# Optimization experiments

Measured on AMD Instinct MI355X. Metric: run time of the kernel, lower is better.

Reference implementation:

```python
import jax, jax.numpy as jnp
import numpy as np

B, S, D_MODEL, N_HEADS, D_K, D_V = 2, 2048, 1024, 16, 64, 64
LN_EPS = 1e-5


def setup_inputs() -> dict:
    key = jax.random.key(0)
    ks = jax.random.split(key, 10)
    scale = 1.0 / np.sqrt(D_MODEL)
    inp = {
        "input_Q": jax.random.normal(ks[0], (B, S, D_MODEL), jnp.float32),
        "input_K": jax.random.normal(ks[1], (B, S, D_MODEL), jnp.float32),
        "input_V": jax.random.normal(ks[2], (B, S, D_MODEL), jnp.float32),
        # causal mask (True = masked), as produced by attn_mask() with no pad tokens
        "attn_mask": jnp.broadcast_to(
            jnp.triu(jnp.ones((S, S), dtype=bool), k=1), (B, S, S)
        ),
        # weights stored [in, out] (equivalent to torch Linear weight.T)
        "W_Q": jax.random.normal(ks[3], (D_MODEL, N_HEADS * D_K), jnp.float32) * scale,
        "W_K": jax.random.normal(ks[4], (D_MODEL, N_HEADS * D_K), jnp.float32) * scale,
        "W_V": jax.random.normal(ks[5], (D_MODEL, N_HEADS * D_V), jnp.float32) * scale,
        "W_O": jax.random.normal(ks[6], (N_HEADS * D_V, D_MODEL), jnp.float32) * scale,
        "ln_gamma": jnp.ones((D_MODEL,), jnp.float32),
        "ln_beta": jnp.zeros((D_MODEL,), jnp.float32),
    }
    return inp


def _layernorm(x, gamma, beta):
    mu = jnp.mean(x, axis=-1, keepdims=True)
    var = jnp.var(x, axis=-1, keepdims=True)
    return (x - mu) * jax.lax.rsqrt(var + LN_EPS) * gamma + beta


def reference(input_Q, input_K, input_V, attn_mask, W_Q, W_K, W_V, W_O, ln_gamma, ln_beta):
    b = input_Q.shape[0]
    # projections -> [B, H, S, d]
    Q = (input_Q @ W_Q).reshape(b, -1, N_HEADS, D_K).transpose(0, 2, 1, 3)
    K = (input_K @ W_K).reshape(b, -1, N_HEADS, D_K).transpose(0, 2, 1, 3)
    V = (input_V @ W_V).reshape(b, -1, N_HEADS, D_V).transpose(0, 2, 1, 3)
    scores = jnp.einsum("bhqd,bhkd->bhqk", Q, K) / np.sqrt(D_K)
    scores = jnp.where(attn_mask[:, None, :, :], jnp.float32(-1e9), scores)
    attn = jax.nn.softmax(scores, axis=-1)
    context = jnp.einsum("bhqk,bhkd->bhqd", attn, V)
    context = context.transpose(0, 2, 1, 3).reshape(b, -1, N_HEADS * D_V)
    output = context @ W_O
    out = _layernorm(output + input_Q, ln_gamma, ln_beta)
    return out, attn
```

## Files before the change

### kernel.cpp

```cpp
#include <hip/hip_runtime.h>
#include <stdint.h>

typedef unsigned short u16;
typedef __attribute__((ext_vector_type(8))) short short8;
typedef __attribute__((ext_vector_type(4))) float f32x4;
typedef __attribute__((ext_vector_type(4))) unsigned short u16x4;
typedef __attribute__((ext_vector_type(4))) unsigned int uint4v;

#define MFMA16(a,b,c) __builtin_amdgcn_mfma_f32_16x16x32_bf16((a),(b),(c),0,0,0)

__device__ __forceinline__ void gload16(const void* g, void* l) {
  __builtin_amdgcn_global_load_lds(
      (__attribute__((address_space(1))) void*)(uintptr_t)(g),
      (__attribute__((address_space(3))) void*)(uint32_t)(uintptr_t)(l),
      16, 0, 0);
}

__device__ __forceinline__ u16 f2bf(float x) {
  union { float f; unsigned u; } v; v.f = x;
  unsigned r = v.u + 0x7fffu + ((v.u >> 16) & 1u);
  return (u16)(r >> 16);
}
__device__ __forceinline__ unsigned pack2(float a, float b) {
  return (unsigned)f2bf(a) | ((unsigned)f2bf(b) << 16);
}

__global__ __launch_bounds__(256) void prep_kernel(const float* x0, const float* x1, const float* x2,
                                                   u16* y0, u16* y1, u16* y2,
                                                   const float* w0, const float* w1, const float* w2, const float* w3,
                                                   u16* t0, u16* t1, u16* t2, u16* t3) {
  __shared__ float tile[32][33];
  int z = blockIdx.y;
  if (z < 3) {
    const float* x = (z == 0) ? x0 : ((z == 1) ? x1 : x2);
    u16*         y = (z == 0) ? y0 : ((z == 1) ? y1 : y2);
    size_t i = ((size_t)blockIdx.x * 256 + threadIdx.x) * 4;
    float4 v = *(const float4*)(x + i);
    u16x4 o; o[0] = f2bf(v.x); o[1] = f2bf(v.y); o[2] = f2bf(v.z); o[3] = f2bf(v.w);
    *(u16x4*)(y + i) = o;
  } else {
    if (blockIdx.x >= 1024) return;
    const float* W; u16* T;
    switch (z - 3) {
      case 0:  W = w0; T = t0; break;
      case 1:  W = w1; T = t1; break;
      case 2:  W = w2; T = t2; break;
      default: W = w3; T = t3; break;
    }
    int k0 = (blockIdx.x >> 5) * 32, n0 = (blockIdx.x & 31) * 32;
    int tx = threadIdx.x & 31, ty = threadIdx.x >> 5;
#pragma unroll
    for (int j = 0; j < 4; ++j)
      tile[ty + 8*j][tx] = W[(size_t)(k0 + ty + 8*j) * 1024 + n0 + tx];
    __syncthreads();
#pragma unroll
    for (int j = 0; j < 4; ++j)
      T[(size_t)(n0 + ty + 8*j) * 1024 + k0 + tx] = f2bf(tile[tx][ty + 8*j]);
  }
}

__device__ __forceinline__ void gemm_stage(const u16* A, const u16* BT, int row0, int col0,
                                           int tid, int w, int kt, char* la, char* lb) {
#pragma unroll
  for (int j = 0; j < 2; ++j) {
    int c = j * 256 + tid;
    int mr = c & 127, kc = c >> 7;
    gload16(A  + (size_t)(row0 + mr) * 1024 + kt*32 + kc*8, la + (j*4 + w) * 1024);
    gload16(BT + (size_t)(col0 + mr) * 1024 + kt*32 + kc*8, lb + (j*4 + w) * 1024);
  }
}

__device__ __forceinline__ void gemm_core(const u16* A, const u16* BT, int row0, int col0,
                                          char* ldsA, char* ldsB, f32x4 (&acc)[4][4]) {
  int tid = threadIdx.x, w = tid >> 6, lane = tid & 63;
  int u = lane >> 4, c16 = lane & 15, wr = w >> 1, wc = w & 1;
  gemm_stage(A, BT, row0, col0, tid, w, 0, ldsA, ldsB);
  gemm_stage(A, BT, row0, col0, tid, w, 1, ldsA + 8192, ldsB + 8192);
  int cur = 0;
  for (int kt = 0; kt < 32; ++kt) {
    if (kt < 31) asm volatile("s_waitcnt vmcnt(4)" ::: "memory");
    else         asm volatile("s_waitcnt vmcnt(0)" ::: "memory");
    __builtin_amdgcn_s_barrier();
    asm volatile("" ::: "memory");
    if (kt < 30) {
      int nb = cur + 2; if (nb >= 3) nb -= 3;
      gemm_stage(A, BT, row0, col0, tid, w, kt + 2, ldsA + nb*8192, ldsB + nb*8192);
    }
    __builtin_amdgcn_sched_barrier(0);
    const char* la = ldsA + cur * 8192;
    const char* lb = ldsB + cur * 8192;
    short8 af[4], bv[4];
#pragma unroll
    for (int i = 0; i < 4; ++i) {
      af[i] = *(const short8*)(la + (u*128 + wr*64 + i*16 + c16) * 16);
      bv[i] = *(const short8*)(lb + (u*128 + wc*64 + i*16 + c16) * 16);
    }
#pragma unroll
    for (int i = 0; i < 4; ++i)
#pragma unroll
      for (int n = 0; n < 4; ++n)
        acc[i][n] = MFMA16(af[i], bv[n], acc[i][n]);
    cur = cur + 1; if (cur >= 3) cur = 0;
  }
}

__global__ __launch_bounds__(256) void gemm_qkv(const u16* Xq, const u16* Xk, const u16* Xv,
                                                const u16* WTq, const u16* WTk, const u16* WTv,
                                                u16* Qh, u16* Kh, u16* VhT) {
  __shared__ char ldsA[24576], ldsB[24576];
  int z = blockIdx.z;
  const u16* A  = (z == 0) ? Xq  : ((z == 1) ? Xk  : Xv);
  const u16* BT = (z == 0) ? WTq : ((z == 1) ? WTk : WTv);
  int row0 = blockIdx.x * 128, col0 = blockIdx.y * 128;
  f32x4 acc[4][4] = {};
  gemm_core(A, BT, row0, col0, ldsA, ldsB, acc);
  int tid = threadIdx.x, w = tid >> 6, lane = tid & 63, u = lane >> 4, c16 = lane & 15;
  int wr = w >> 1, wc = w & 1;
#pragma unroll
  for (int i = 0; i < 4; ++i)
#pragma unroll
    for (int n = 0; n < 4; ++n)
#pragma unroll
      for (int r = 0; r < 4; ++r) {
        int row = row0 + wr*64 + i*16 + u*4 + r;
        int colg = col0 + wc*64 + n*16 + c16;
        int b = row >> 11, s = row & 2047;
        int h = colg >> 6, d = colg & 63;
        float v = acc[i][n][r];
        if (z == 0)      Qh[((size_t)(b*16 + h) * 2048 + s) * 64 + d] = f2bf(v * 0.125f);
        else if (z == 1) Kh[((size_t)(b*16 + h) * 2048 + s) * 64 + d] = f2bf(v);
        else             VhT[((size_t)(b*16 + h) * 64 + d) * 2048 + s] = f2bf(v);
      }
}

__global__ __launch_bounds__(256) void gemm_out(const u16* Ctx, const u16* WTo,
                                                const float* resid, float* outF) {
  __shared__ char ldsA[24576], ldsB[24576];
  int row0 = blockIdx.x * 128, col0 = blockIdx.y * 128;
  f32x4 acc[4][4] = {};
  gemm_core(Ctx, WTo, row0, col0, ldsA, ldsB, acc);
  int tid = threadIdx.x, w = tid >> 6, lane = tid & 63, u = lane >> 4, c16 = lane & 15;
  int wr = w >> 1, wc = w & 1;
#pragma unroll
  for (int i = 0; i < 4; ++i)
#pragma unroll
    for (int n = 0; n < 4; ++n)
#pragma unroll
      for (int r = 0; r < 4; ++r) {
        int row = row0 + wr*64 + i*16 + u*4 + r;
        int colg = col0 + wc*64 + n*16 + c16;
        size_t idx = (size_t)row * 1024 + colg;
        outF[idx] = acc[i][n][r] + resid[idx];
      }
}

__device__ __forceinline__ void qk_tile(const char* Kbuf, short8 qf0, short8 qf1,
                                        int cq, int u, int rho, f32x4 (&acc)[4]) {
#pragma unroll
  for (int st = 0; st < 4; ++st) {
    short8 a0 = *(const short8*)(Kbuf + (st*16 + cq) * 128 + ((u*16) ^ rho));
    short8 a1 = *(const short8*)(Kbuf + (st*16 + cq) * 128 + ((64 + u*16) ^ rho));
    acc[st] = MFMA16(a0, qf0, acc[st]);
    acc[st] = MFMA16(a1, qf1, acc[st]);
  }
}

__device__ __forceinline__ void stage_k64(const u16* pan, int kt, char* buf, int tid, int w) {
#pragma unroll
  for (int j = 0; j < 2; ++j) {
    int c = j * 256 + tid;
    int row = c >> 3;
    int cc = (c & 7) ^ (row & 7);
    gload16(pan + (size_t)(kt*64 + row) * 64 + cc*8, buf + (j*4 + w) * 1024);
  }
}
__device__ __forceinline__ void stage_v64(const u16* vpan, int kt, char* buf, int tid, int w) {
#pragma unroll
  for (int j = 0; j < 2; ++j) {
    int c = j * 256 + tid;
    int d = c >> 3;
    int cc = (c & 7) ^ (d & 7);
    gload16(vpan + (size_t)d * 2048 + kt*64 + cc*8, buf + (j*4 + w) * 1024);
  }
}

__device__ __forceinline__ void tile_pass1(const char* Kcur, short8 qf0, short8 qf1,
                                           int q, int q0t, int kt, int ktd_t,
                                           int cq, int u, int rho, float& ls) {
  f32x4 acc[4] = {};
  qk_tile(Kcur, qf0, qf1, cq, u, rho, acc);
  if (kt == ktd_t) {
#pragma unroll
    for (int st = 0; st < 4; ++st)
#pragma unroll
      for (int r = 0; r < 4; ++r) {
        int key = q0t + st*16 + u*4 + r;
        if (key > q) acc[st][r] = -1e30f;
      }
  }
#pragma unroll
  for (int st = 0; st < 4; ++st)
#pragma unroll
    for (int r = 0; r < 4; ++r) ls += __expf(acc[st][r]);
}

__device__ __forceinline__ void tile_pass2(const char* Kcur, const char* Vcur, float* Pw,
                                           short8 qf0, short8 qf1, int q, int q0t, int kt, int ktd_t,
                                           float rl, float* apan, int w, int u, int cq,
                                           int rho, int sw, f32x4 (&ctx)[4]) {
  f32x4 acc[4] = {};
  __builtin_amdgcn_s_setprio(1);
  qk_tile(Kcur, qf0, qf1, cq, u, rho, acc);
  if (kt == ktd_t) {
#pragma unroll
    for (int st = 0; st < 4; ++st)
#pragma unroll
      for (int r = 0; r < 4; ++r) {
        int key = q0t + st*16 + u*4 + r;
        if (key > q) acc[st][r] = -1e30f;
      }
  }
#pragma unroll
  for (int st = 0; st < 4; ++st) {
    f32x4 p;
#pragma unroll
    for (int r = 0; r < 4; ++r) p[r] = __expf(acc[st][r]) * rl;
    *(f32x4*)&Pw[(cq*64 + st*16 + u*4) ^ sw] = p;
  }
  __builtin_amdgcn_sched_barrier(0);
#pragma unroll
  for (int j = 0; j < 4; ++j) {
    int row = j*4 + u;
    f32x4 v = *(const f32x4*)&Pw[(row*64 + cq*4) ^ ((row & 7) << 2)];
    __builtin_nontemporal_store(v,
        (f32x4*)(apan + (size_t)(q0t + w*16 + row) * 2048 + kt*64 + cq*4));
  }
#pragma unroll
  for (int wd = 0; wd < 2; ++wd) {
    int b0 = (cq*64 + wd*32 + u*8) ^ sw;
    f32x4 pa0 = *(const f32x4*)&Pw[b0];
    f32x4 pa1 = *(const f32x4*)&Pw[b0 ^ 4];
    uint4v pk;
    pk[0] = pack2(pa0[0], pa0[1]);
    pk[1] = pack2(pa0[2], pa0[3]);
    pk[2] = pack2(pa1[0], pa1[1]);
    pk[3] = pack2(pa1[2], pa1[3]);
    union { uint4v u4; short8 s8; } cvt; cvt.u4 = pk;
    short8 pa = cvt.s8;
#pragma unroll
    for (int nt = 0; nt < 4; ++nt) {
      short8 vb = *(const short8*)(Vcur + (nt*16 + cq) * 128 + ((wd*64 + u*16) ^ rho));
      ctx[nt] = MFMA16(pa, vb, ctx[nt]);
    }
  }
  __builtin_amdgcn_s_setprio(0);
  __builtin_amdgcn_sched_barrier(0);
}

__global__ __launch_bounds__(256) void attn_fused(const u16* Qh, const u16* Kh, const u16* VhT,
                                                  float* attnO, u16* Ctx) {
  __shared__ char Kl[2][8192];
  __shared__ char Vl[2][8192];
  __shared__ float Pf[4][1024];
  int tid = threadIdx.x, w = tid >> 6, lane = tid & 63;
  int u = lane >> 4, cq = lane & 15;
  int pi = blockIdx.x;
  int bh = blockIdx.y;
  int tlo = pi, thi = 31 - pi;
  int q0lo = tlo * 64, q0hi = thi * 64;
  int qlo = q0lo + w*16 + cq;
  int qhi = q0hi + w*16 + cq;
  int rho = (cq & 7) << 4;
  int sw  = (cq & 7) << 2;
  const u16* Kpan = Kh  + (size_t)bh * (2048 * 64);
  const u16* Vpan = VhT + (size_t)bh * (64 * 2048);
  const u16* Qlo = Qh + ((size_t)bh * 2048 + qlo) * 64;
  const u16* Qhi = Qh + ((size_t)bh * 2048 + qhi) * 64;
  short8 qlo0 = *(const short8*)(Qlo + u*8);
  short8 qlo1 = *(const short8*)(Qlo + 32 + u*8);
  short8 qhi0 = *(const short8*)(Qhi + u*8);
  short8 qhi1 = *(const short8*)(Qhi + 32 + u*8);
  float* apan = attnO + (size_t)bh * 2048 * 2048;
  int nlo = 31 - tlo;
  f32x4 z4 = {};

  float ls_lo = 0.f, ls_hi = 0.f;
  stage_k64(Kpan, 0, Kl[0], tid, w);
  for (int kt = 0; kt <= thi; ++kt) {
    int cur = kt & 1;
    if (kt == 0 || kt > 16)  asm volatile("s_waitcnt vmcnt(0)" ::: "memory");
    else if (kt <= 15)       asm volatile("s_waitcnt vmcnt(8)" ::: "memory");
    else                     asm volatile("s_waitcnt vmcnt(4)" ::: "memory");
    __builtin_amdgcn_s_barrier();
    asm volatile("" ::: "memory");
    if (kt < thi) stage_k64(Kpan, kt + 1, Kl[cur ^ 1], tid, w);
    int ns = (kt < 15) ? 8 : ((kt == 15) ? 4 : 0);
    for (int s = 0; s < ns; ++s) {
      int zidx = kt * 8 + s;
      int t = zidx >> 2, j = zidx & 3;
      int ktz, q0t;
      if (t < nlo) { ktz = tlo + 1 + t;         q0t = q0lo; }
      else         { ktz = thi + 1 + (t - nlo); q0t = q0hi; }
      __builtin_nontemporal_store(z4,
          (f32x4*)(apan + (size_t)(q0t + w*16 + j*4 + u) * 2048 + ktz*64 + cq*4));
    }
    __builtin_amdgcn_sched_barrier(0);
    __builtin_amdgcn_s_setprio(1);
    tile_pass1(Kl[cur], qhi0, qhi1, qhi, q0hi, kt, thi, cq, u, rho, ls_hi);
    if (kt <= tlo)
      tile_pass1(Kl[cur], qlo0, qlo1, qlo, q0lo, kt, tlo, cq, u, rho, ls_lo);
    __builtin_amdgcn_s_setprio(0);
  }
  ls_lo += __shfl_xor(ls_lo, 16);  ls_lo += __shfl_xor(ls_lo, 32);
  ls_hi += __shfl_xor(ls_hi, 16);  ls_hi += __shfl_xor(ls_hi, 32);
  float rl_lo = 1.f / ls_lo, rl_hi = 1.f / ls_hi;

  asm volatile("" ::: "memory");
  __builtin_amdgcn_s_barrier();
  asm volatile("" ::: "memory");

  f32x4 ctx_lo[4] = {}, ctx_hi[4] = {};
  float* Pw = Pf[w];
  stage_k64(Kpan, 0, Kl[0], tid, w);
  stage_v64(Vpan, 0, Vl[0], tid, w);
  asm volatile("s_waitcnt vmcnt(0)" ::: "memory");
  __builtin_amdgcn_s_barrier();
  asm volatile("" ::: "memory");
  for (int kt = 0; kt <= thi; ++kt) {
    int cur = kt & 1;
    if (kt < thi) {
      stage_k64(Kpan, kt + 1, Kl[cur ^ 1], tid, w);
      stage_v64(Vpan, kt + 1, Vl[cur ^ 1], tid, w);
    }
    __builtin_amdgcn_sched_barrier(0);
    tile_pass2(Kl[cur], Vl[cur], Pw, qhi0, qhi1, qhi, q0hi, kt, thi,
               rl_hi, apan, w, u, cq, rho, sw, ctx_hi);
    bool lo_act = (kt <= tlo);
    if (lo_act)
      tile_pass2(Kl[cur], Vl[cur], Pw, qlo0, qlo1, qlo, q0lo, kt, tlo,
                 rl_lo, apan, w, u, cq, rho, sw, ctx_lo);
    if (kt < thi) {
      if (lo_act) asm volatile("s_waitcnt vmcnt(8)" ::: "memory");
      else        asm volatile("s_waitcnt vmcnt(4)" ::: "memory");
      __builtin_amdgcn_s_barrier();
      asm volatile("" ::: "memory");
    }
  }

  int b = bh >> 4, h = bh & 15;
#pragma unroll
  for (int nt = 0; nt < 4; ++nt)
#pragma unroll
    for (int r = 0; r < 4; ++r) {
      int qr = q0lo + w*16 + u*4 + r;
      Ctx[((size_t)b * 2048 + qr) * 1024 + h*64 + nt*16 + cq] = f2bf(ctx_lo[nt][r]);
    }
#pragma unroll
  for (int nt = 0; nt < 4; ++nt)
#pragma unroll
    for (int r = 0; r < 4; ++r) {
      int qr = q0hi + w*16 + u*4 + r;
      Ctx[((size_t)b * 2048 + qr) * 1024 + h*64 + nt*16 + cq] = f2bf(ctx_hi[nt][r]);
    }
}

__global__ __launch_bounds__(256) void ln_kernel(const float* X, const float* g, const float* b, float* out) {
  int row = blockIdx.x, tid = threadIdx.x;
  float4 v = *(const float4*)(X + (size_t)row * 1024 + tid * 4);
  float s  = v.x + v.y + v.z + v.w;
  float q2 = v.x*v.x + v.y*v.y + v.z*v.z + v.w*v.w;
#pragma unroll
  for (int off = 32; off; off >>= 1) { s += __shfl_xor(s, off); q2 += __shfl_xor(q2, off); }
  __shared__ float red[8];
  int w = tid >> 6, lane = tid & 63;
  if (lane == 0) { red[w] = s; red[4 + w] = q2; }
  __syncthreads();
  s  = red[0] + red[1] + red[2] + red[3];
  q2 = red[4] + red[5] + red[6] + red[7];
  float mean = s * (1.f / 1024.f);
  float var  = q2 * (1.f / 1024.f) - mean * mean;
  float rs   = rsqrtf(var + 1e-5f);
  float4 gv = *(const float4*)(g + tid * 4);
  float4 bv = *(const float4*)(b + tid * 4);
  float4 o;
  o.x = (v.x - mean) * rs * gv.x + bv.x;
  o.y = (v.y - mean) * rs * gv.y + bv.y;
  o.z = (v.z - mean) * rs * gv.z + bv.z;
  o.w = (v.w - mean) * rs * gv.w + bv.w;
  *(float4*)(out + (size_t)row * 1024 + tid * 4) = o;
}

extern "C" void kernel_launch(void* const* d_in, const int* in_sizes, int n_in,
                              void* d_out, int out_size, void* d_ws, size_t ws_size,
                              hipStream_t stream) {
  (void)in_sizes; (void)n_in; (void)out_size; (void)ws_size;
  const float* inQ = (const float*)d_in[0];
  const float* inK = (const float*)d_in[1];
  const float* inV = (const float*)d_in[2];
  const float* Wq  = (const float*)d_in[4];
  const float* Wk  = (const float*)d_in[5];
  const float* Wv  = (const float*)d_in[6];
  const float* Wo  = (const float*)d_in[7];
  const float* gam = (const float*)d_in[8];
  const float* bet = (const float*)d_in[9];
  float* out   = (float*)d_out;
  float* attnO = out + (size_t)4194304;

  char* ws = (char*)d_ws;
  u16*   WTo    = (u16*)ws;
  u16*   Qh     = (u16*)(ws + 2097152);
  u16*   Kh     = (u16*)(ws + 2097152 + (size_t)8388608);
  u16*   VhT    = (u16*)(ws + 2097152 + (size_t)2*8388608);
  u16*   Ctx    = (u16*)(ws + 2097152 + (size_t)3*8388608);
  float* OutLin = (float*)(ws + 2097152 + (size_t)4*8388608);

  u16* Xbq = (u16*)attnO;
  u16* Xbk = Xbq + (size_t)4194304;
  u16* Xbv = Xbk + (size_t)4194304;
  u16* WTq = Xbv + (size_t)4194304;
  u16* WTk = WTq + (size_t)1048576;
  u16* WTv = WTk + (size_t)1048576;

  prep_kernel<<<dim3(4096, 7), 256, 0, stream>>>(inQ, inK, inV, Xbq, Xbk, Xbv,
                                                 Wq, Wk, Wv, Wo, WTq, WTk, WTv, WTo);
  gemm_qkv<<<dim3(32, 8, 3), 256, 0, stream>>>(Xbq, Xbk, Xbv, WTq, WTk, WTv, Qh, Kh, VhT);
  attn_fused<<<dim3(16, 32), 256, 0, stream>>>(Qh, Kh, VhT, attnO, Ctx);
  gemm_out<<<dim3(32, 8), 256, 0, stream>>>(Ctx, WTo, inQ, OutLin);
  ln_kernel<<<4096, 256, 0, stream>>>(OutLin, gam, bet, out);
}
```

Baseline: 270.8 us.

## Split softmax row-sum pass into separate kernel and triple-buffer attention loads

The first pass of the fused attention kernel (row sums of exp of scores, plus zero-filling the masked attn region) moves into its own kernel that writes row sums to a workspace buffer. The second pass reads those sums and now uses a three-stage K/V buffer with prefetch two tiles ahead, using computed vmcnt waits. The QKV GEMM also writes the transposed V output as packed 4-element vector stores. The aim is shorter per-kernel critical paths and better latency hiding. The cost is an extra launch, a second read of Q and K, and more LDS, which may lower occupancy.

After: 287.1 us. +6.0%, slower.

```diff
diff --git a/kernel.cpp b/kernel.cpp
--- a/kernel.cpp
+++ b/kernel.cpp
@@ -8,6 +8,7 @@
 typedef __attribute__((ext_vector_type(4))) unsigned int uint4v;
 
 #define MFMA16(a,b,c) __builtin_amdgcn_mfma_f32_16x16x32_bf16((a),(b),(c),0,0,0)
+#define VWAIT(n) asm volatile("s_waitcnt vmcnt(" #n ")" ::: "memory")
 
 __device__ __forceinline__ void gload16(const void* g, void* l) {
   __builtin_amdgcn_global_load_lds(
@@ -78,8 +79,8 @@
   gemm_stage(A, BT, row0, col0, tid, w, 1, ldsA + 8192, ldsB + 8192);
   int cur = 0;
   for (int kt = 0; kt < 32; ++kt) {
-    if (kt < 31) asm volatile("s_waitcnt vmcnt(4)" ::: "memory");
-    else         asm volatile("s_waitcnt vmcnt(0)" ::: "memory");
+    if (kt < 31) VWAIT(4);
+    else         VWAIT(0);
     __builtin_amdgcn_s_barrier();
     asm volatile("" ::: "memory");
     if (kt < 30) {
@@ -116,21 +117,36 @@
   gemm_core(A, BT, row0, col0, ldsA, ldsB, acc);
   int tid = threadIdx.x, w = tid >> 6, lane = tid & 63, u = lane >> 4, c16 = lane & 15;
   int wr = w >> 1, wc = w & 1;
-#pragma unroll
-  for (int i = 0; i < 4; ++i)
-#pragma unroll
-    for (int n = 0; n < 4; ++n)
-#pragma unroll
-      for (int r = 0; r < 4; ++r) {
-        int row = row0 + wr*64 + i*16 + u*4 + r;
+  if (z == 2) {
+#pragma unroll
+    for (int i = 0; i < 4; ++i)
+#pragma unroll
+      for (int n = 0; n < 4; ++n) {
+        int rowb = row0 + wr*64 + i*16 + u*4;
         int colg = col0 + wc*64 + n*16 + c16;
-        int b = row >> 11, s = row & 2047;
+        int b = rowb >> 11, s = rowb & 2047;
         int h = colg >> 6, d = colg & 63;
-        float v = acc[i][n][r];
-        if (z == 0)      Qh[((size_t)(b*16 + h) * 2048 + s) * 64 + d] = f2bf(v * 0.125f);
-        else if (z == 1) Kh[((size_t)(b*16 + h) * 2048 + s) * 64 + d] = f2bf(v);
-        else             VhT[((size_t)(b*16 + h) * 64 + d) * 2048 + s] = f2bf(v);
+        u16x4 pv;
+#pragma unroll
+        for (int r = 0; r < 4; ++r) pv[r] = f2bf(acc[i][n][r]);
+        *(u16x4*)(VhT + ((size_t)(b*16 + h) * 64 + d) * 2048 + s) = pv;
       }
+  } else {
+#pragma unroll
+    for (int i = 0; i < 4; ++i)
+#pragma unroll
+      for (int n = 0; n < 4; ++n)
+#pragma unroll
+        for (int r = 0; r < 4; ++r) {
+          int row = row0 + wr*64 + i*16 + u*4 + r;
+          int colg = col0 + wc*64 + n*16 + c16;
+          int b = row >> 11, s = row & 2047;
+          int h = colg >> 6, d = colg & 63;
+          float v = acc[i][n][r];
+          if (z == 0) Qh[((size_t)(b*16 + h) * 2048 + s) * 64 + d] = f2bf(v * 0.125f);
+          else        Kh[((size_t)(b*16 + h) * 2048 + s) * 64 + d] = f2bf(v);
+        }
+  }
 }
 
 __global__ __launch_bounds__(256) void gemm_out(const u16* Ctx, const u16* WTo,
@@ -184,9 +200,9 @@
   }
 }
 
-__device__ __forceinline__ void tile_pass1(const char* Kcur, short8 qf0, short8 qf1,
-                                           int q, int q0t, int kt, int ktd_t,
-                                           int cq, int u, int rho, float& ls) {
+__device__ __forceinline__ void tile_sum(const char* Kcur, short8 qf0, short8 qf1,
+                                         int q, int q0t, int kt, int ktd_t,
+                                         int cq, int u, int rho, float& ls) {
   f32x4 acc[4] = {};
   qk_tile(Kcur, qf0, qf1, cq, u, rho, acc);
   if (kt == ktd_t) {
@@ -202,6 +218,71 @@
   for (int st = 0; st < 4; ++st)
 #pragma unroll
     for (int r = 0; r < 4; ++r) ls += __expf(acc[st][r]);
+}
+
+__global__ __launch_bounds__(256) void sumexp_kernel(const u16* Qh, const u16* Kh,
+                                                     float* lsum, float* attnO) {
+  __shared__ char Kl[3][8192];
+  int tid = threadIdx.x, w = tid >> 6, lane = tid & 63;
+  int u = lane >> 4, cq = lane & 15;
+  int pi = blockIdx.x, bh = blockIdx.y;
+  int tlo = pi, thi = 31 - pi;
+  int q0lo = tlo * 64, q0hi = thi * 64;
+  int qlo = q0lo + w*16 + cq, qhi = q0hi + w*16 + cq;
+  int rho = (cq & 7) << 4;
+  const u16* Kpan = Kh + (size_t)bh * (2048 * 64);
+  const u16* Qlo = Qh + ((size_t)bh * 2048 + qlo) * 64;
+  const u16* Qhi = Qh + ((size_t)bh * 2048 + qhi) * 64;
+  short8 qlo0 = *(const short8*)(Qlo + u*8);
+  short8 qlo1 = *(const short8*)(Qlo + 32 + u*8);
+  short8 qhi0 = *(const short8*)(Qhi + u*8);
+  short8 qhi1 = *(const short8*)(Qhi + 32 + u*8);
+  float* apan = attnO + (size_t)bh * 2048 * 2048;
+  int nlo = 31 - tlo;
+  f32x4 z4 = {};
+  float ls_lo = 0.f, ls_hi = 0.f;
+
+  stage_k64(Kpan, 0, Kl[0], tid, w);
+  stage_k64(Kpan, 1, Kl[1], tid, w);
+  for (int kt = 0; kt <= thi; ++kt) {
+    int cur = kt % 3;
+    if (kt == 0)            VWAIT(2);
+    else if (kt == 1)       VWAIT(10);
+    else if (kt <= 15)      VWAIT(18);
+    else if (kt == 16)      { if (thi == 16) VWAIT(12); else VWAIT(14); }
+    else if (kt == 17)      { if (thi == 17) VWAIT(4);  else VWAIT(6); }
+    else if (kt < thi)      VWAIT(2);
+    else                    VWAIT(0);
+    __builtin_amdgcn_s_barrier();
+    asm volatile("" ::: "memory");
+    if (kt + 2 <= thi) {
+      int nb = (kt + 2) % 3;
+      stage_k64(Kpan, kt + 2, Kl[nb], tid, w);
+    }
+    __builtin_amdgcn_sched_barrier(0);
+    int ns = (kt < 15) ? 8 : ((kt == 15) ? 4 : 0);
+    for (int s = 0; s < ns; ++s) {
+      int zidx = kt * 8 + s;
+      int t = zidx >> 2, j = zidx & 3;
+      int ktz, q0t;
+      if (t < nlo) { ktz = tlo + 1 + t;         q0t = q0lo; }
+      else         { ktz = thi + 1 + (t - nlo); q0t = q0hi; }
+      __builtin_nontemporal_store(z4,
+          (f32x4*)(apan + (size_t)(q0t + w*16 + j*4 + u) * 2048 + ktz*64 + cq*4));
+    }
+    __builtin_amdgcn_sched_barrier(0);
+    __builtin_amdgcn_s_setprio(1);
+    tile_sum(Kl[cur], qhi0, qhi1, qhi, q0hi, kt, thi, cq, u, rho, ls_hi);
+    if (kt <= tlo)
+      tile_sum(Kl[cur], qlo0, qlo1, qlo, q0lo, kt, tlo, cq, u, rho, ls_lo);
+    __builtin_amdgcn_s_setprio(0);
+  }
+  ls_lo += __shfl_xor(ls_lo, 16);  ls_lo += __shfl_xor(ls_lo, 32);
+  ls_hi += __shfl_xor(ls_hi, 16);  ls_hi += __shfl_xor(ls_hi, 32);
+  if (u == 0) {
+    lsum[(size_t)bh * 2048 + qlo] = ls_lo;
+    lsum[(size_t)bh * 2048 + qhi] = ls_hi;
+  }
 }
 
 __device__ __forceinline__ void tile_pass2(const char* Kcur, const char* Vcur, float* Pw,
@@ -258,14 +339,13 @@
 }
 
 __global__ __launch_bounds__(256) void attn_fused(const u16* Qh, const u16* Kh, const u16* VhT,
-                                                  float* attnO, u16* Ctx) {
-  __shared__ char Kl[2][8192];
-  __shared__ char Vl[2][8192];
+                                                  const float* lsum, float* attnO, u16* Ctx) {
+  __shared__ char Kl[3][8192];
+  __shared__ char Vl[3][8192];
   __shared__ float Pf[4][1024];
   int tid = threadIdx.x, w = tid >> 6, lane = tid & 63;
   int u = lane >> 4, cq = lane & 15;
-  int pi = blockIdx.x;
-  int bh = blockIdx.y;
+  int pi = blockIdx.x, bh = blockIdx.y;
   int tlo = pi, thi = 31 - pi;
   int q0lo = tlo * 64, q0hi = thi * 64;
   int qlo = q0lo + w*16 + cq;
@@ -280,71 +360,43 @@
   short8 qlo1 = *(const short8*)(Qlo + 32 + u*8);
   short8 qhi0 = *(const short8*)(Qhi + u*8);
   short8 qhi1 = *(const short8*)(Qhi + 32 + u*8);
+  float rl_lo = 1.f / lsum[(size_t)bh * 2048 + qlo];
+  float rl_hi = 1.f / lsum[(size_t)bh * 2048 + qhi];
   float* apan = attnO + (size_t)bh * 2048 * 2048;
-  int nlo = 31 - tlo;
-  f32x4 z4 = {};
-
-  float ls_lo = 0.f, ls_hi = 0.f;
+  float* Pw = Pf[w];
+  f32x4 ctx_lo[4] = {}, ctx_hi[4] = {};
+
   stage_k64(Kpan, 0, Kl[0], tid, w);
+  stage_v64(Vpan, 0, Vl[0], tid, w);
+  stage_k64(Kpan, 1, Kl[1], tid, w);
+  stage_v64(Vpan, 1, Vl[1], tid, w);
   for (int kt = 0; kt <= thi; ++kt) {
-    int cur = kt & 1;
-    if (kt == 0 || kt > 16)  asm volatile("s_waitcnt vmcnt(0)" ::: "memory");
-    else if (kt <= 15)       asm volatile("s_waitcnt vmcnt(8)" ::: "memory");
-    else                     asm volatile("s_waitcnt vmcnt(4)" ::: "memory");
+    int cur = kt % 3;
+    if (kt == 0)      VWAIT(4);
+    else if (kt == 1) VWAIT(12);
+    else {
+      int a  = (kt-2 <= tlo) ? 8 : 4;
+      int b2 = (kt-1 <= tlo) ? 8 : 4;
+      int c  = (kt+1 <= thi) ? 4 : 0;
+      int N = a + b2 + c;
+      if (N == 20)      VWAIT(20);
+      else if (N == 16) VWAIT(16);
+      else if (N == 12) VWAIT(12);
+      else              VWAIT(8);
+    }
     __builtin_amdgcn_s_barrier();
     asm volatile("" ::: "memory");
-    if (kt < thi) stage_k64(Kpan, kt + 1, Kl[cur ^ 1], tid, w);
-    int ns = (kt < 15) ? 8 : ((kt == 15) ? 4 : 0);
-    for (int s = 0; s < ns; ++s) {
-      int zidx = kt * 8 + s;
-      int t = zidx >> 2, j = zidx & 3;
-      int ktz, q0t;
-      if (t < nlo) { ktz = tlo + 1 + t;         q0t = q0lo; }
-      else         { ktz = thi + 1 + (t - nlo); q0t = q0hi; }
-      __builtin_nontemporal_store(z4,
-          (f32x4*)(apan + (size_t)(q0t + w*16 + j*4 + u) * 2048 + ktz*64 + cq*4));
-    }
-    __builtin_amdgcn_sched_barrier(0);
-    __builtin_amdgcn_s_setprio(1);
-    tile_pass1(Kl[cur], qhi0, qhi1, qhi, q0hi, kt, thi, cq, u, rho, ls_hi);
-    if (kt <= tlo)
-      tile_pass1(Kl[cur], qlo0, qlo1, qlo, q0lo, kt, tlo, cq, u, rho, ls_lo);
-    __builtin_amdgcn_s_setprio(0);
-  }
-  ls_lo += __shfl_xor(ls_lo, 16);  ls_lo += __shfl_xor(ls_lo, 32);
-  ls_hi += __shfl_xor(ls_hi, 16);  ls_hi += __shfl_xor(ls_hi, 32);
-  float rl_lo = 1.f / ls_lo, rl_hi = 1.f / ls_hi;
-
-  asm volatile("" ::: "memory");
-  __builtin_amdgcn_s_barrier();
-  asm volatile("" ::: "memory");
-
-  f32x4 ctx_lo[4] = {}, ctx_hi[4] = {};
-  float* Pw = Pf[w];
-  stage_k64(Kpan, 0, Kl[0], tid, w);
-  stage_v64(Vpan, 0, Vl[0], tid, w);
-  asm volatile("s_waitcnt vmcnt(0)" ::: "memory");
-  __builtin_amdgcn_s_barrier();
-  asm volatile("" ::: "memory");
-  for (int kt = 0; kt <= thi; ++kt) {
-    int cur = kt & 1;
-    if (kt < thi) {
-      stage_k64(Kpan, kt + 1, Kl[cur ^ 1], tid, w);
-      stage_v64(Vpan, kt + 1, Vl[cur ^ 1], tid, w);
+    if (kt + 2 <= thi) {
+      int nb = (kt + 2) % 3;
+      stage_k64(Kpan, kt + 2, Kl[nb], tid, w);
+      stage_v64(Vpan, kt + 2, Vl[nb], tid, w);
     }
     __builtin_amdgcn_sched_barrier(0);
     tile_pass2(Kl[cur], Vl[cur], Pw, qhi0, qhi1, qhi, q0hi, kt, thi,
                rl_hi, apan, w, u, cq, rho, sw, ctx_hi);
-    bool lo_act = (kt <= tlo);
-    if (lo_act)
+    if (kt <= tlo)
       tile_pass2(Kl[cur], Vl[cur], Pw, qlo0, qlo1, qlo, q0lo, kt, tlo,
                  rl_lo, apan, w, u, cq, rho, sw, ctx_lo);
-    if (kt < thi) {
-      if (lo_act) asm volatile("s_waitcnt vmcnt(8)" ::: "memory");
-      else        asm volatile("s_waitcnt vmcnt(4)" ::: "memory");
-      __builtin_amdgcn_s_barrier();
-      asm volatile("" ::: "memory");
-    }
   }
 
   int b = bh >> 4, h = bh & 15;
@@ -412,7 +464,8 @@
   u16*   Kh     = (u16*)(ws + 2097152 + (size_t)8388608);
   u16*   VhT    = (u16*)(ws + 2097152 + (size_t)2*8388608);
   u16*   Ctx    = (u16*)(ws + 2097152 + (size_t)3*8388608);
-  float* OutLin = (float*)(ws + 2097152 + (size_t)4*8388608);
+  float* lsum   = (float*)(ws + 2097152 + (size_t)4*8388608);
+  float* OutLin = (float*)(ws + 2097152 + (size_t)4*8388608 + 262144);
 
   u16* Xbq = (u16*)attnO;
   u16* Xbk = Xbq + (size_t)4194304;
@@ -424,7 +477,8 @@
   prep_kernel<<<dim3(4096, 7), 256, 0, stream>>>(inQ, inK, inV, Xbq, Xbk, Xbv,
                                                  Wq, Wk, Wv, Wo, WTq, WTk, WTv, WTo);
   gemm_qkv<<<dim3(32, 8, 3), 256, 0, stream>>>(Xbq, Xbk, Xbv, WTq, WTk, WTv, Qh, Kh, VhT);
-  attn_fused<<<dim3(16, 32), 256, 0, stream>>>(Qh, Kh, VhT, attnO, Ctx);
+  sumexp_kernel<<<dim3(16, 32), 256, 0, stream>>>(Qh, Kh, lsum, attnO);
+  attn_fused<<<dim3(16, 32), 256, 0, stream>>>(Qh, Kh, VhT, lsum, attnO, Ctx);
   gemm_out<<<dim3(32, 8), 256, 0, stream>>>(Ctx, WTo, inQ, OutLin);
   ln_kernel<<<4096, 256, 0, stream>>>(OutLin, gam, bet, out);
 }
```
